# Optimization experiments

Measured on AMD Instinct MI355X. Metric: run time of the kernel, lower is better.

Reference implementation:

```python
import jax, jax.numpy as jnp
import numpy as np

B, T, C = 1, 2048, 3072
H, HKV, D = 24, 8, 128          # heads, kv heads, head_dim
G = H // HKV                    # gqa groups = 3
ROPE_BASE = 10000.0


def _rope_cos_sin(seq_len, dim, dtype):
    inv_freq = 1.0 / (ROPE_BASE ** (jnp.arange(0, dim, 2, dtype=jnp.float32) / dim))
    t = jnp.arange(seq_len, dtype=jnp.float32)
    freqs = t[:, None] * inv_freq[None, :]            # [T, D/2]
    emb = jnp.concatenate([freqs, freqs], axis=-1)    # [T, D]
    return jnp.cos(emb).astype(dtype), jnp.sin(emb).astype(dtype)


def _rotate_half(x):
    h = x.shape[-1] // 2
    return jnp.concatenate([-x[..., h:], x[..., :h]], axis=-1)


def setup_inputs() -> dict:
    key = jax.random.key(0)
    ks = jax.random.split(key, 5)
    s = 0.02
    return {
        "x":  jax.random.normal(ks[0], (B, T, C), dtype=jnp.float32),
        "Wq": jax.random.normal(ks[1], (C, H * D), dtype=jnp.float32) * s,
        "Wk": jax.random.normal(ks[2], (C, HKV * D), dtype=jnp.float32) * s,
        "Wv": jax.random.normal(ks[3], (C, HKV * D), dtype=jnp.float32) * s,
        "Wo": jax.random.normal(ks[4], (C, C), dtype=jnp.float32) * s,
    }


def reference(x, Wq, Wk, Wv, Wo):
    b, t, c = x.shape
    # projections -> [B, H(or HKV), T, D]
    q = (x @ Wq).reshape(b, t, H, D).transpose(0, 2, 1, 3)
    k = (x @ Wk).reshape(b, t, HKV, D).transpose(0, 2, 1, 3)
    v = (x @ Wv).reshape(b, t, HKV, D).transpose(0, 2, 1, 3)
    # GQA: repeat_interleave kv heads to full head count
    k = jnp.repeat(k, G, axis=1)
    v = jnp.repeat(v, G, axis=1)
    # RoPE
    cos, sin = _rope_cos_sin(t, D, x.dtype)           # [T, D]
    cos = cos[None, None]                             # [1,1,T,D]
    sin = sin[None, None]
    q = q * cos + _rotate_half(q) * sin
    k = k * cos + _rotate_half(k) * sin
    # causal SDPA
    scale = 1.0 / jnp.sqrt(jnp.asarray(D, dtype=x.dtype))
    scores = jnp.einsum('bhqd,bhkd->bhqk', q, k) * scale
    causal = jnp.tril(jnp.ones((t, t), dtype=bool))
    scores = jnp.where(causal[None, None], scores, jnp.finfo(x.dtype).min)
    attn = jax.nn.softmax(scores, axis=-1)
    out = jnp.einsum('bhqk,bhkd->bhqd', attn, v)      # [B,H,T,D]
    out = out.transpose(0, 2, 1, 3).reshape(b, t, c)
    return out @ Wo
```

## Files before the change

kernel.cpp:

```cpp
#include <hip/hip_runtime.h>
#include <cstdint>

#define T_SEQ 2048
#define C_DIM 3072
#define NH    24
#define NKV   8
#define HD    128
#define N_TILES (32 * 24)

typedef short  bf16x8 __attribute__((ext_vector_type(8)));
typedef float  f32x4  __attribute__((ext_vector_type(4)));

__device__ __forceinline__ ushort f2bf(float f) {
    union { float f; uint32_t u; } v; v.f = f;
    uint32_t r = (v.u + 0x7FFF + ((v.u >> 16) & 1)) >> 16;
    return (ushort)r;
}

__device__ __forceinline__ uint32_t cvtpk_bf16(float lo, float hi) {
    uint32_t r;
    asm("v_cvt_pk_bf16_f32 %0, %1, %2" : "=v"(r) : "v"(lo), "v"(hi));
    return r;
}

__device__ __forceinline__ float fast_exp2(float x) {
#if __has_builtin(__builtin_amdgcn_exp2f)
    return __builtin_amdgcn_exp2f(x);
#else
    return exp2f(x);
#endif
}

__device__ __forceinline__ void gll16(const void* g, void* lds) {
    __builtin_amdgcn_global_load_lds(
        (const __attribute__((address_space(1))) uint32_t*)g,
        (__attribute__((address_space(3))) uint32_t*)lds, 16, 0, 0);
}

__global__ void zero_ctr(int* c) { *c = 0; }

__global__ __launch_bounds__(64) void rope_table(float* __restrict__ cosT,
                                                 float* __restrict__ sinT) {
    int t = blockIdx.x;
    int j = threadIdx.x;
    float inv = powf(10000.0f, -(float)j * (1.0f / 64.0f));
    float ang = (float)t * inv;
    cosT[t * 64 + j] = cosf(ang);
    sinT[t * 64 + j] = sinf(ang);
}

__global__ __launch_bounds__(256) void convert_x(const float* __restrict__ x,
                                                 ushort* __restrict__ xb) {
    int i = blockIdx.x * 256 + threadIdx.x;
    int stride = gridDim.x * 256;
    const int n4 = (T_SEQ * C_DIM) / 4;
    for (; i < n4; i += stride) {
        float4 v = ((const float4*)x)[i];
        ushort4 o;
        o.x = f2bf(v.x); o.y = f2bf(v.y); o.z = f2bf(v.z); o.w = f2bf(v.w);
        ((ushort4*)xb)[i] = o;
    }
}

__global__ __launch_bounds__(256) void transpose_w(const float* __restrict__ src,
                                                   ushort* __restrict__ dst,
                                                   int ldN) {
    __shared__ float sT[64][65];
    const int n0 = blockIdx.x * 64;
    const int k0 = blockIdx.y * 64;
    const int r  = threadIdx.x >> 4;
    const int c4 = (threadIdx.x & 15) * 4;
    #pragma unroll
    for (int i = 0; i < 4; ++i) {
        int kk = r + i * 16;
        float4 v = *(const float4*)&src[(size_t)(k0 + kk) * ldN + n0 + c4];
        sT[kk][c4 + 0] = v.x; sT[kk][c4 + 1] = v.y;
        sT[kk][c4 + 2] = v.z; sT[kk][c4 + 3] = v.w;
    }
    __syncthreads();
    #pragma unroll
    for (int i = 0; i < 4; ++i) {
        int nn = r + i * 16;
        ushort4 o;
        o.x = f2bf(sT[c4 + 0][nn]); o.y = f2bf(sT[c4 + 1][nn]);
        o.z = f2bf(sT[c4 + 2][nn]); o.w = f2bf(sT[c4 + 3][nn]);
        *(ushort4*)&dst[(size_t)(n0 + nn) * C_DIM + k0 + c4] = o;
    }
}

__global__ __launch_bounds__(256) void qkv_gemm_mfma(
    const ushort* __restrict__ xb, const ushort* __restrict__ WbT,
    const float* __restrict__ cosT, const float* __restrict__ sinT,
    ushort* __restrict__ Qb, ushort* __restrict__ Kb, ushort* __restrict__ Vt) {

    __shared__ ushort sA[128 * 64];
    __shared__ ushort sB[128 * 64];

    const int bid = (int)blockIdx.x;
    const int swzb = (bid & 7) * 80 + (bid >> 3);
    const int bx = swzb % 40;
    const int by = swzb / 40;
    const int tid = threadIdx.x;
    const int w = tid >> 6, l = tid & 63, g = l >> 4, c = l & 15;
    const int m0 = by * 128, n0 = bx * 128;

    f32x4 acc[2][8];
    #pragma unroll
    for (int m = 0; m < 2; ++m)
        #pragma unroll
        for (int n = 0; n < 8; ++n) acc[m][n] = {0.f, 0.f, 0.f, 0.f};

    const int ch = (w * 4) * 64 + l;
    for (int k0 = 0; k0 < C_DIM; k0 += 64) {
        __syncthreads();
        #pragma unroll
        for (int u = 0; u < 4; ++u) {
            int chu = ch + u * 64;
            int row = chu >> 3, sub = chu & 7;
            int sc  = sub ^ (row & 7);
            gll16(xb  + (size_t)(m0 + row) * C_DIM + k0 + sc * 8, &sA[(w * 4 + u) * 512]);
            gll16(WbT + (size_t)(n0 + row) * C_DIM + k0 + sc * 8, &sB[(w * 4 + u) * 512]);
        }
        __syncthreads();

        #pragma unroll
        for (int kc = 0; kc < 2; ++kc) {
            bf16x8 a[2], b[8];
            #pragma unroll
            for (int m = 0; m < 2; ++m) {
                int row = w * 32 + m * 16 + c;
                int chp = (kc * 4 + g) ^ (row & 7);
                a[m] = *(const bf16x8*)&sA[row * 64 + chp * 8];
            }
            #pragma unroll
            for (int n = 0; n < 8; ++n) {
                int row = n * 16 + c;
                int chp = (kc * 4 + g) ^ (row & 7);
                b[n] = *(const bf16x8*)&sB[row * 64 + chp * 8];
            }
            #pragma unroll
            for (int m = 0; m < 2; ++m)
                #pragma unroll
                for (int n = 0; n < 8; ++n)
                    acc[m][n] = __builtin_amdgcn_mfma_f32_16x16x32_bf16(a[m], b[n], acc[m][n], 0, 0, 0);
        }
    }

    if (bx < 32) {
        const bool isQ = (bx < 24);
        const float qscl = isQ ? (0.08838834764831845f * 1.4426950408889634f) : 1.0f;
        ushort* dst = isQ ? (Qb + (size_t)bx * T_SEQ * HD)
                          : (Kb + (size_t)(bx - 24) * T_SEQ * HD);
        #pragma unroll
        for (int m = 0; m < 2; ++m) {
            #pragma unroll
            for (int n = 0; n < 4; ++n) {
                #pragma unroll
                for (int r = 0; r < 4; ++r) {
                    int t = m0 + w * 32 + m * 16 + g * 4 + r;
                    int d = n * 16 + c;
                    float q1 = acc[m][n][r] * qscl, q2 = acc[m][n + 4][r] * qscl;
                    float cv = cosT[t * 64 + d], sv = sinT[t * 64 + d];
                    dst[(size_t)t * HD + d]      = f2bf(q1 * cv - q2 * sv);
                    dst[(size_t)t * HD + 64 + d] = f2bf(q2 * cv + q1 * sv);
                }
            }
        }
    } else {
        ushort* dst = Vt + (size_t)(bx - 32) * HD * T_SEQ;
        #pragma unroll
        for (int m = 0; m < 2; ++m) {
            #pragma unroll
            for (int n = 0; n < 8; ++n) {
                int d  = n * 16 + c;
                int t0 = m0 + w * 32 + m * 16 + g * 4;
                ushort4 pk;
                pk.x = f2bf(acc[m][n][0]); pk.y = f2bf(acc[m][n][1]);
                pk.z = f2bf(acc[m][n][2]); pk.w = f2bf(acc[m][n][3]);
                *(ushort4*)&dst[(size_t)d * T_SEQ + t0] = pk;
            }
        }
    }
}

__global__ __launch_bounds__(256) void attn_mfma(
    const ushort* __restrict__ Qb, const ushort* __restrict__ Kb,
    const ushort* __restrict__ Vt, ushort* __restrict__ AO,
    int* __restrict__ ctr) {

    __shared__ ushort sK[2][64 * 128];
    __shared__ ushort sV[2][128 * 64];
    __shared__ ushort sP[4][16][72];
    __shared__ int s_tile;

    const int tid = threadIdx.x;
    const int w = tid >> 6, l = tid & 63, g = l >> 4, c = l & 15;

    for (;;) {
        if (tid == 0) s_tile = atomicAdd(ctr, 1);
        __syncthreads();
        const int tau = s_tile;
        if (tau >= N_TILES) break;
        const int qt = 31 - tau / 24;
        const int h  = tau % 24;
        const int kh = h / 3;

        const ushort* Qp = Qb + (size_t)h  * T_SEQ * HD;
        const ushort* Kp = Kb + (size_t)kh * T_SEQ * HD;
        const ushort* Vp = Vt + (size_t)kh * HD * T_SEQ;

        const int myq = qt * 64 + w * 16 + c;
        bf16x8 qf[4];
        #pragma unroll
        for (int kc = 0; kc < 4; ++kc)
            qf[kc] = *(const bf16x8*)&Qp[(size_t)myq * HD + kc * 32 + g * 8];

        f32x4 o[8];
        #pragma unroll
        for (int n = 0; n < 8; ++n) o[n] = {0.f, 0.f, 0.f, 0.f};
        float m_run = -3.0e38f, l_run = 0.f;

        #define STAGE_KV(ktile, buf)                                                 \
            {                                                                        \
                _Pragma("unroll")                                                    \
                for (int u = 0; u < 4; ++u) {                                        \
                    int chunk = (w * 4 + u) * 64 + l;                                \
                    int row = chunk >> 4;                                            \
                    int sub = (chunk & 15) ^ (row & 7);                              \
                    gll16(Kp + (size_t)((ktile) * 64 + row) * HD + sub * 8,          \
                          &sK[buf][(w * 4 + u) * 512]);                              \
                }                                                                    \
                _Pragma("unroll")                                                    \
                for (int u = 0; u < 4; ++u) {                                        \
                    int chunk = (w * 4 + u) * 64 + l;                                \
                    int row = chunk >> 3;                                            \
                    int sub = (chunk & 7) ^ (row & 7);                               \
                    gll16(Vp + (size_t)row * T_SEQ + (ktile) * 64 + sub * 8,         \
                          &sV[buf][(w * 4 + u) * 512]);                              \
                }                                                                    \
            }

        int cur = 0;
        STAGE_KV(0, 0);
        __syncthreads();

        for (int kt = 0; kt <= qt; ++kt) {
            if (kt < qt) STAGE_KV(kt + 1, cur ^ 1);

            f32x4 sacc[4];
            #pragma unroll
            for (int nt = 0; nt < 4; ++nt) sacc[nt] = {0.f, 0.f, 0.f, 0.f};
            const ushort* sKc = &sK[cur][0];
            __builtin_amdgcn_s_setprio(1);
            #pragma unroll
            for (int nt = 0; nt < 4; ++nt) {
                int row = nt * 16 + c;
                #pragma unroll
                for (int kc = 0; kc < 4; ++kc) {
                    int chp = (kc * 4 + g) ^ (row & 7);
                    bf16x8 kf = *(const bf16x8*)&sKc[row * 128 + chp * 8];
                    sacc[nt] = __builtin_amdgcn_mfma_f32_16x16x32_bf16(kf, qf[kc], sacc[nt], 0, 0, 0);
                }
            }
            __builtin_amdgcn_s_setprio(0);

            float p[16];
            float pm = -3.0e38f;
            #pragma unroll
            for (int nt = 0; nt < 4; ++nt) {
                #pragma unroll
                for (int r = 0; r < 4; ++r) {
                    int key = kt * 64 + nt * 16 + g * 4 + r;
                    float s = sacc[nt][r];
                    s = (key > myq) ? -3.0e38f : s;
                    p[nt * 4 + r] = s;
                    pm = fmaxf(pm, s);
                }
            }
            pm = fmaxf(pm, __shfl_xor(pm, 16));
            pm = fmaxf(pm, __shfl_xor(pm, 32));

            if (!__all(pm <= m_run + 8.0f)) {
                float mnew = fmaxf(m_run, pm);
                float alpha = fast_exp2(m_run - mnew);
                m_run = mnew;
                l_run *= alpha;
                float aR[4];
                #pragma unroll
                for (int r = 0; r < 4; ++r) aR[r] = __shfl(alpha, g * 4 + r);
                #pragma unroll
                for (int n = 0; n < 8; ++n) {
                    f32x4 t = o[n];
                    t[0] *= aR[0]; t[1] *= aR[1]; t[2] *= aR[2]; t[3] *= aR[3];
                    o[n] = t;
                }
            }
            float psum = 0.f;
            #pragma unroll
            for (int i = 0; i < 16; ++i) {
                float e = fast_exp2(p[i] - m_run);
                p[i] = e;
                psum += e;
            }
            psum += __shfl_xor(psum, 16);
            psum += __shfl_xor(psum, 32);
            l_run += psum;

            #pragma unroll
            for (int nt = 0; nt < 4; ++nt) {
                uint2 v;
                v.x = cvtpk_bf16(p[nt * 4 + 0], p[nt * 4 + 1]);
                v.y = cvtpk_bf16(p[nt * 4 + 2], p[nt * 4 + 3]);
                *(uint2*)&sP[w][c][nt * 16 + g * 4] = v;
            }

            const ushort* sVc = &sV[cur][0];
            __builtin_amdgcn_s_setprio(1);
            #pragma unroll
            for (int kc2 = 0; kc2 < 2; ++kc2) {
                bf16x8 pa = *(const bf16x8*)&sP[w][c][kc2 * 32 + g * 8];
                #pragma unroll
                for (int n = 0; n < 8; ++n) {
                    int row = n * 16 + c;
                    int chp = (kc2 * 4 + g) ^ (row & 7);
                    bf16x8 vf = *(const bf16x8*)&sVc[row * 64 + chp * 8];
                    o[n] = __builtin_amdgcn_mfma_f32_16x16x32_bf16(pa, vf, o[n], 0, 0, 0);
                }
            }
            __builtin_amdgcn_s_setprio(0);

            __syncthreads();
            cur ^= 1;
        }
        #undef STAGE_KV

        float invR[4];
        #pragma unroll
        for (int r = 0; r < 4; ++r) invR[r] = 1.0f / __shfl(l_run, g * 4 + r);
        #pragma unroll
        for (int n = 0; n < 8; ++n)
            #pragma unroll
            for (int r = 0; r < 4; ++r) {
                int t = qt * 64 + w * 16 + g * 4 + r;
                AO[(size_t)t * C_DIM + h * HD + n * 16 + c] = f2bf(o[n][r] * invR[r]);
            }
    }
}

__global__ __launch_bounds__(256) void out_gemm_mfma(
    const ushort* __restrict__ Ab, const ushort* __restrict__ BT,
    float* __restrict__ outp) {

    __shared__ ushort sA[128 * 64];
    __shared__ ushort sB[128 * 64];

    const int bid = (int)blockIdx.x;
    const int swzb = (bid & 7) * 48 + (bid >> 3);
    const int bx = swzb % 24;
    const int by = swzb / 24;
    const int tid = threadIdx.x;
    const int w = tid >> 6, l = tid & 63, g = l >> 4, c = l & 15;
    const int m0 = by * 128, n0 = bx * 128;

    f32x4 acc[2][8];
    #pragma unroll
    for (int m = 0; m < 2; ++m)
        #pragma unroll
        for (int n = 0; n < 8; ++n) acc[m][n] = {0.f, 0.f, 0.f, 0.f};

    const int ch = (w * 4) * 64 + l;
    for (int k0 = 0; k0 < C_DIM; k0 += 64) {
        __syncthreads();
        #pragma unroll
        for (int u = 0; u < 4; ++u) {
            int chu = ch + u * 64;
            int row = chu >> 3, sub = chu & 7;
            int sc  = sub ^ (row & 7);
            gll16(Ab + (size_t)(m0 + row) * C_DIM + k0 + sc * 8, &sA[(w * 4 + u) * 512]);
            gll16(BT + (size_t)(n0 + row) * C_DIM + k0 + sc * 8, &sB[(w * 4 + u) * 512]);
        }
        __syncthreads();

        #pragma unroll
        for (int kc = 0; kc < 2; ++kc) {
            bf16x8 a[2], b[8];
            #pragma unroll
            for (int m = 0; m < 2; ++m) {
                int row = w * 32 + m * 16 + c;
                int chp = (kc * 4 + g) ^ (row & 7);
                a[m] = *(const bf16x8*)&sA[row * 64 + chp * 8];
            }
            #pragma unroll
            for (int n = 0; n < 8; ++n) {
                int row = n * 16 + c;
                int chp = (kc * 4 + g) ^ (row & 7);
                b[n] = *(const bf16x8*)&sB[row * 64 + chp * 8];
            }
            #pragma unroll
            for (int m = 0; m < 2; ++m)
                #pragma unroll
                for (int n = 0; n < 8; ++n)
                    acc[m][n] = __builtin_amdgcn_mfma_f32_16x16x32_bf16(a[m], b[n], acc[m][n], 0, 0, 0);
        }
    }

    #pragma unroll
    for (int m = 0; m < 2; ++m)
        #pragma unroll
        for (int n = 0; n < 8; ++n)
            #pragma unroll
            for (int r = 0; r < 4; ++r) {
                int t = m0 + w * 32 + m * 16 + g * 4 + r;
                outp[(size_t)t * C_DIM + n0 + n * 16 + c] = acc[m][n][r];
            }
}

extern "C" void kernel_launch(void* const* d_in, const int* in_sizes, int n_in,
                              void* d_out, int out_size, void* d_ws, size_t ws_size,
                              hipStream_t stream) {
    const float* x  = (const float*)d_in[0];
    const float* Wq = (const float*)d_in[1];
    const float* Wk = (const float*)d_in[2];
    const float* Wv = (const float*)d_in[3];
    const float* Wo = (const float*)d_in[4];

    char* ws = (char*)d_ws;
    int*    ctr  = (int*)ws;                           ws += 256;
    float*  cosT = (float*)ws;                         ws += 2048 * 64 * 4;
    float*  sinT = (float*)ws;                         ws += 2048 * 64 * 4;
    ushort* WbT  = (ushort*)ws;                        ws += (size_t)5120 * 3072 * 2;
    ushort* WoT  = (ushort*)ws;                        ws += (size_t)3072 * 3072 * 2;
    ushort* Qb   = (ushort*)ws;                        ws += (size_t)NH  * T_SEQ * HD * 2;
    ushort* Kb   = (ushort*)ws;                        ws += (size_t)NKV * T_SEQ * HD * 2;
    ushort* Vt   = (ushort*)ws;                        ws += (size_t)NKV * T_SEQ * HD * 2;
    ushort* xb   = (ushort*)ws;
    ushort* AO   = xb;
    float*  out  = (float*)d_out;

    zero_ctr   <<<dim3(1),      dim3(1),   0, stream>>>(ctr);
    rope_table <<<dim3(2048),   dim3(64),  0, stream>>>(cosT, sinT);
    convert_x  <<<dim3(2048),   dim3(256), 0, stream>>>(x, xb);
    transpose_w<<<dim3(48, 48), dim3(256), 0, stream>>>(Wq, WbT,                       3072);
    transpose_w<<<dim3(16, 48), dim3(256), 0, stream>>>(Wk, WbT + (size_t)3072 * 3072, 1024);
    transpose_w<<<dim3(16, 48), dim3(256), 0, stream>>>(Wv, WbT + (size_t)4096 * 3072, 1024);
    transpose_w<<<dim3(48, 48), dim3(256), 0, stream>>>(Wo, WoT,                       3072);

    qkv_gemm_mfma<<<dim3(640), dim3(256), 0, stream>>>(xb, WbT, cosT, sinT, Qb, Kb, Vt);
    attn_mfma    <<<dim3(512), dim3(256), 0, stream>>>(Qb, Kb, Vt, AO, ctr);
    out_gemm_mfma<<<dim3(384), dim3(256), 0, stream>>>(AO, WoT, out);
}
```

Measured before the change: 407.2 us.

## Fuse prep kernels and halve GEMM M-tile to raise block count

Merges counter zeroing, RoPE table and x conversion into one prep kernel, and the four weight transposes into one launch, cutting launch overhead. Both projection GEMMs move from 128x128 to 64x128 tiles, doubling grid size (1280 and 768 blocks) so more of the CUs stay busy. The cost is lower arithmetic intensity per tile, since each B tile is reused across only 16 rows per wave, which means more LDS and global traffic per MFMA.

```diff
diff --git a/kernel.cpp b/kernel.cpp
--- a/kernel.cpp
+++ b/kernel.cpp
@@ -37,24 +37,23 @@
         (__attribute__((address_space(3))) uint32_t*)lds, 16, 0, 0);
 }
 
-__global__ void zero_ctr(int* c) { *c = 0; }
-
-__global__ __launch_bounds__(64) void rope_table(float* __restrict__ cosT,
-                                                 float* __restrict__ sinT) {
-    int t = blockIdx.x;
-    int j = threadIdx.x;
-    float inv = powf(10000.0f, -(float)j * (1.0f / 64.0f));
-    float ang = (float)t * inv;
-    cosT[t * 64 + j] = cosf(ang);
-    sinT[t * 64 + j] = sinf(ang);
-}
-
-__global__ __launch_bounds__(256) void convert_x(const float* __restrict__ x,
-                                                 ushort* __restrict__ xb) {
-    int i = blockIdx.x * 256 + threadIdx.x;
-    int stride = gridDim.x * 256;
+__global__ __launch_bounds__(256) void prep(const float* __restrict__ x,
+                                            ushort* __restrict__ xb,
+                                            float* __restrict__ cosT,
+                                            float* __restrict__ sinT,
+                                            int* __restrict__ ctr) {
+    const int t = blockIdx.x;
+    const int tid = threadIdx.x;
+    if (t == 0 && tid == 0) *ctr = 0;
+    if (tid < 64) {
+        float inv = powf(10000.0f, -(float)tid * (1.0f / 64.0f));
+        float ang = (float)t * inv;
+        cosT[t * 64 + tid] = cosf(ang);
+        sinT[t * 64 + tid] = sinf(ang);
+    }
     const int n4 = (T_SEQ * C_DIM) / 4;
-    for (; i < n4; i += stride) {
+    const int stride = gridDim.x * 256;
+    for (int i = t * 256 + tid; i < n4; i += stride) {
         float4 v = ((const float4*)x)[i];
         ushort4 o;
         o.x = f2bf(v.x); o.y = f2bf(v.y); o.z = f2bf(v.z); o.w = f2bf(v.w);
@@ -62,11 +61,20 @@
     }
 }
 
-__global__ __launch_bounds__(256) void transpose_w(const float* __restrict__ src,
-                                                   ushort* __restrict__ dst,
-                                                   int ldN) {
+__global__ __launch_bounds__(256) void transpose_all(
+    const float* __restrict__ Wq, const float* __restrict__ Wk,
+    const float* __restrict__ Wv, const float* __restrict__ Wo,
+    ushort* __restrict__ WbT, ushort* __restrict__ WoT) {
+
     __shared__ float sT[64][65];
-    const int n0 = blockIdx.x * 64;
+    const int bx = blockIdx.x;
+    const float* src; ushort* dst; int ldN, nstrip;
+    if (bx < 48)      { src = Wq; dst = WbT;                       ldN = 3072; nstrip = bx; }
+    else if (bx < 64) { src = Wk; dst = WbT + (size_t)3072 * 3072; ldN = 1024; nstrip = bx - 48; }
+    else if (bx < 80) { src = Wv; dst = WbT + (size_t)4096 * 3072; ldN = 1024; nstrip = bx - 64; }
+    else              { src = Wo; dst = WoT;                       ldN = 3072; nstrip = bx - 80; }
+
+    const int n0 = nstrip * 64;
     const int k0 = blockIdx.y * 64;
     const int r  = threadIdx.x >> 4;
     const int c4 = (threadIdx.x & 15) * 4;
@@ -93,56 +101,51 @@
     const float* __restrict__ cosT, const float* __restrict__ sinT,
     ushort* __restrict__ Qb, ushort* __restrict__ Kb, ushort* __restrict__ Vt) {
 
-    __shared__ ushort sA[128 * 64];
+    __shared__ ushort sA[64 * 64];
     __shared__ ushort sB[128 * 64];
 
-    const int bid = (int)blockIdx.x;
-    const int swzb = (bid & 7) * 80 + (bid >> 3);
+    const int bid  = (int)blockIdx.x;
+    const int swzb = (bid & 7) * 160 + (bid >> 3);
+    const int by = swzb / 40;
     const int bx = swzb % 40;
-    const int by = swzb / 40;
     const int tid = threadIdx.x;
     const int w = tid >> 6, l = tid & 63, g = l >> 4, c = l & 15;
-    const int m0 = by * 128, n0 = bx * 128;
-
-    f32x4 acc[2][8];
+    const int m0 = by * 64, n0 = bx * 128;
+
+    f32x4 acc[8];
     #pragma unroll
-    for (int m = 0; m < 2; ++m)
-        #pragma unroll
-        for (int n = 0; n < 8; ++n) acc[m][n] = {0.f, 0.f, 0.f, 0.f};
-
-    const int ch = (w * 4) * 64 + l;
+    for (int n = 0; n < 8; ++n) acc[n] = {0.f, 0.f, 0.f, 0.f};
+
     for (int k0 = 0; k0 < C_DIM; k0 += 64) {
         __syncthreads();
         #pragma unroll
-        for (int u = 0; u < 4; ++u) {
-            int chu = ch + u * 64;
+        for (int u = 0; u < 2; ++u) {
+            int chu = (w * 2 + u) * 64 + l;
             int row = chu >> 3, sub = chu & 7;
             int sc  = sub ^ (row & 7);
-            gll16(xb  + (size_t)(m0 + row) * C_DIM + k0 + sc * 8, &sA[(w * 4 + u) * 512]);
+            gll16(xb + (size_t)(m0 + row) * C_DIM + k0 + sc * 8, &sA[(w * 2 + u) * 512]);
+        }
+        #pragma unroll
+        for (int u = 0; u < 4; ++u) {
+            int chu = (w * 4 + u) * 64 + l;
+            int row = chu >> 3, sub = chu & 7;
+            int sc  = sub ^ (row & 7);
             gll16(WbT + (size_t)(n0 + row) * C_DIM + k0 + sc * 8, &sB[(w * 4 + u) * 512]);
         }
         __syncthreads();
 
         #pragma unroll
         for (int kc = 0; kc < 2; ++kc) {
-            bf16x8 a[2], b[8];
-            #pragma unroll
-            for (int m = 0; m < 2; ++m) {
-                int row = w * 32 + m * 16 + c;
-                int chp = (kc * 4 + g) ^ (row & 7);
-                a[m] = *(const bf16x8*)&sA[row * 64 + chp * 8];
-            }
+            int arow = w * 16 + c;
+            int achp = (kc * 4 + g) ^ (arow & 7);
+            bf16x8 av = *(const bf16x8*)&sA[arow * 64 + achp * 8];
             #pragma unroll
             for (int n = 0; n < 8; ++n) {
-                int row = n * 16 + c;
-                int chp = (kc * 4 + g) ^ (row & 7);
-                b[n] = *(const bf16x8*)&sB[row * 64 + chp * 8];
-            }
-            #pragma unroll
-            for (int m = 0; m < 2; ++m)
-                #pragma unroll
-                for (int n = 0; n < 8; ++n)
-                    acc[m][n] = __builtin_amdgcn_mfma_f32_16x16x32_bf16(a[m], b[n], acc[m][n], 0, 0, 0);
+                int brow = n * 16 + c;
+                int chp  = (kc * 4 + g) ^ (brow & 7);
+                bf16x8 bv = *(const bf16x8*)&sB[brow * 64 + chp * 8];
+                acc[n] = __builtin_amdgcn_mfma_f32_16x16x32_bf16(av, bv, acc[n], 0, 0, 0);
+            }
         }
     }
 
@@ -152,33 +155,27 @@
         ushort* dst = isQ ? (Qb + (size_t)bx * T_SEQ * HD)
                           : (Kb + (size_t)(bx - 24) * T_SEQ * HD);
         #pragma unroll
-        for (int m = 0; m < 2; ++m) {
-            #pragma unroll
-            for (int n = 0; n < 4; ++n) {
-                #pragma unroll
-                for (int r = 0; r < 4; ++r) {
-                    int t = m0 + w * 32 + m * 16 + g * 4 + r;
-                    int d = n * 16 + c;
-                    float q1 = acc[m][n][r] * qscl, q2 = acc[m][n + 4][r] * qscl;
-                    float cv = cosT[t * 64 + d], sv = sinT[t * 64 + d];
-                    dst[(size_t)t * HD + d]      = f2bf(q1 * cv - q2 * sv);
-                    dst[(size_t)t * HD + 64 + d] = f2bf(q2 * cv + q1 * sv);
-                }
+        for (int n = 0; n < 4; ++n) {
+            #pragma unroll
+            for (int r = 0; r < 4; ++r) {
+                int t = m0 + w * 16 + g * 4 + r;
+                int d = n * 16 + c;
+                float q1 = acc[n][r] * qscl, q2 = acc[n + 4][r] * qscl;
+                float cv = cosT[t * 64 + d], sv = sinT[t * 64 + d];
+                dst[(size_t)t * HD + d]      = f2bf(q1 * cv - q2 * sv);
+                dst[(size_t)t * HD + 64 + d] = f2bf(q2 * cv + q1 * sv);
             }
         }
     } else {
         ushort* dst = Vt + (size_t)(bx - 32) * HD * T_SEQ;
         #pragma unroll
-        for (int m = 0; m < 2; ++m) {
-            #pragma unroll
-            for (int n = 0; n < 8; ++n) {
-                int d  = n * 16 + c;
-                int t0 = m0 + w * 32 + m * 16 + g * 4;
-                ushort4 pk;
-                pk.x = f2bf(acc[m][n][0]); pk.y = f2bf(acc[m][n][1]);
-                pk.z = f2bf(acc[m][n][2]); pk.w = f2bf(acc[m][n][3]);
-                *(ushort4*)&dst[(size_t)d * T_SEQ + t0] = pk;
-            }
+        for (int n = 0; n < 8; ++n) {
+            int d  = n * 16 + c;
+            int t0 = m0 + w * 16 + g * 4;
+            ushort4 pk;
+            pk.x = f2bf(acc[n][0]); pk.y = f2bf(acc[n][1]);
+            pk.z = f2bf(acc[n][2]); pk.w = f2bf(acc[n][3]);
+            *(ushort4*)&dst[(size_t)d * T_SEQ + t0] = pk;
         }
     }
 }
@@ -351,68 +348,61 @@
     const ushort* __restrict__ Ab, const ushort* __restrict__ BT,
     float* __restrict__ outp) {
 
-    __shared__ ushort sA[128 * 64];
+    __shared__ ushort sA[64 * 64];
     __shared__ ushort sB[128 * 64];
 
-    const int bid = (int)blockIdx.x;
-    const int swzb = (bid & 7) * 48 + (bid >> 3);
+    const int bid  = (int)blockIdx.x;
+    const int swzb = (bid & 7) * 96 + (bid >> 3);
+    const int by = swzb / 24;
     const int bx = swzb % 24;
-    const int by = swzb / 24;
     const int tid = threadIdx.x;
     const int w = tid >> 6, l = tid & 63, g = l >> 4, c = l & 15;
-    const int m0 = by * 128, n0 = bx * 128;
-
-    f32x4 acc[2][8];
+    const int m0 = by * 64, n0 = bx * 128;
+
+    f32x4 acc[8];
     #pragma unroll
-    for (int m = 0; m < 2; ++m)
-        #pragma unroll
-        for (int n = 0; n < 8; ++n) acc[m][n] = {0.f, 0.f, 0.f, 0.f};
-
-    const int ch = (w * 4) * 64 + l;
+    for (int n = 0; n < 8; ++n) acc[n] = {0.f, 0.f, 0.f, 0.f};
+
     for (int k0 = 0; k0 < C_DIM; k0 += 64) {
         __syncthreads();
         #pragma unroll
-        for (int u = 0; u < 4; ++u) {
-            int chu = ch + u * 64;
+        for (int u = 0; u < 2; ++u) {
+            int chu = (w * 2 + u) * 64 + l;
             int row = chu >> 3, sub = chu & 7;
             int sc  = sub ^ (row & 7);
-            gll16(Ab + (size_t)(m0 + row) * C_DIM + k0 + sc * 8, &sA[(w * 4 + u) * 512]);
+            gll16(Ab + (size_t)(m0 + row) * C_DIM + k0 + sc * 8, &sA[(w * 2 + u) * 512]);
+        }
+        #pragma unroll
+        for (int u = 0; u < 4; ++u) {
+            int chu = (w * 4 + u) * 64 + l;
+            int row = chu >> 3, sub = chu & 7;
+            int sc  = sub ^ (row & 7);
             gll16(BT + (size_t)(n0 + row) * C_DIM + k0 + sc * 8, &sB[(w * 4 + u) * 512]);
         }
         __syncthreads();
 
         #pragma unroll
         for (int kc = 0; kc < 2; ++kc) {
-            bf16x8 a[2], b[8];
-            #pragma unroll
-            for (int m = 0; m < 2; ++m) {
-                int row = w * 32 + m * 16 + c;
-                int chp = (kc * 4 + g) ^ (row & 7);
-                a[m] = *(const bf16x8*)&sA[row * 64 + chp * 8];
-            }
+            int arow = w * 16 + c;
+            int achp = (kc * 4 + g) ^ (arow & 7);
+            bf16x8 av = *(const bf16x8*)&sA[arow * 64 + achp * 8];
             #pragma unroll
             for (int n = 0; n < 8; ++n) {
-                int row = n * 16 + c;
-                int chp = (kc * 4 + g) ^ (row & 7);
-                b[n] = *(const bf16x8*)&sB[row * 64 + chp * 8];
-            }
-            #pragma unroll
-            for (int m = 0; m < 2; ++m)
-                #pragma unroll
-                for (int n = 0; n < 8; ++n)
-                    acc[m][n] = __builtin_amdgcn_mfma_f32_16x16x32_bf16(a[m], b[n], acc[m][n], 0, 0, 0);
+                int brow = n * 16 + c;
+                int chp  = (kc * 4 + g) ^ (brow & 7);
+                bf16x8 bv = *(const bf16x8*)&sB[brow * 64 + chp * 8];
+                acc[n] = __builtin_amdgcn_mfma_f32_16x16x32_bf16(av, bv, acc[n], 0, 0, 0);
+            }
         }
     }
 
     #pragma unroll
-    for (int m = 0; m < 2; ++m)
-        #pragma unroll
-        for (int n = 0; n < 8; ++n)
-            #pragma unroll
-            for (int r = 0; r < 4; ++r) {
-                int t = m0 + w * 32 + m * 16 + g * 4 + r;
-                outp[(size_t)t * C_DIM + n0 + n * 16 + c] = acc[m][n][r];
-            }
+    for (int n = 0; n < 8; ++n)
+        #pragma unroll
+        for (int r = 0; r < 4; ++r) {
+            int t = m0 + w * 16 + g * 4 + r;
+            outp[(size_t)t * C_DIM + n0 + n * 16 + c] = acc[n][r];
+        }
 }
 
 extern "C" void kernel_launch(void* const* d_in, const int* in_sizes, int n_in,
@@ -437,15 +427,9 @@
     ushort* AO   = xb;
     float*  out  = (float*)d_out;
 
-    zero_ctr   <<<dim3(1),      dim3(1),   0, stream>>>(ctr);
-    rope_table <<<dim3(2048),   dim3(64),  0, stream>>>(cosT, sinT);
-    convert_x  <<<dim3(2048),   dim3(256), 0, stream>>>(x, xb);
-    transpose_w<<<dim3(48, 48), dim3(256), 0, stream>>>(Wq, WbT,                       3072);
-    transpose_w<<<dim3(16, 48), dim3(256), 0, stream>>>(Wk, WbT + (size_t)3072 * 3072, 1024);
-    transpose_w<<<dim3(16, 48), dim3(256), 0, stream>>>(Wv, WbT + (size_t)4096 * 3072, 1024);
-    transpose_w<<<dim3(48, 48), dim3(256), 0, stream>>>(Wo, WoT,                       3072);
-
-    qkv_gemm_mfma<<<dim3(640), dim3(256), 0, stream>>>(xb, WbT, cosT, sinT, Qb, Kb, Vt);
-    attn_mfma    <<<dim3(512), dim3(256), 0, stream>>>(Qb, Kb, Vt, AO, ctr);
-    out_gemm_mfma<<<dim3(384), dim3(256), 0, stream>>>(AO, WoT, out);
-}
+    prep         <<<dim3(2048),    dim3(256), 0, stream>>>(x, xb, cosT, sinT, ctr);
+    transpose_all<<<dim3(128, 48), dim3(256), 0, stream>>>(Wq, Wk, Wv, Wo, WbT, WoT);
+    qkv_gemm_mfma<<<dim3(1280),    dim3(256), 0, stream>>>(xb, WbT, cosT, sinT, Qb, Kb, Vt);
+    attn_mfma    <<<dim3(512),     dim3(256), 0, stream>>>(Qb, Kb, Vt, AO, ctr);
+    out_gemm_mfma<<<dim3(768),     dim3(256), 0, stream>>>(AO, WoT, out);
+}
```

Result: faster. 385.4 us (-5.3%).
